# Kernel optimization log

Measured on AMD Instinct MI355X. Metric: run time of the kernel, lower is better.

Reference implementation:

```python
import jax, jax.numpy as jnp
import numpy as np

N, E = 50000, 800000
IN_C, OUT_C, HEADS = 128, 16, 8
EDGE_DIM = 1
NEG_SLOPE = 0.2
LN_EPS = 1e-5


def setup_inputs() -> dict:
    key = jax.random.key(0)
    ks = jax.random.split(key, 12)
    s = 1.0 / np.sqrt(IN_C)
    HC = OUT_C * HEADS
    return {
        "x": jax.random.normal(ks[0], (N, IN_C), jnp.float32),
        "edge_index": jax.random.randint(ks[1], (2, E), 0, N, jnp.int32),
        "edge_attr": jax.random.normal(ks[2], (E, EDGE_DIM), jnp.float32),
        "W": jax.random.normal(ks[3], (IN_C, HC), jnp.float32) * s,
        "b": jnp.zeros((HC,), jnp.float32),
        "att_src": jax.random.normal(ks[4], (HEADS, OUT_C), jnp.float32) * s,
        "att_dst": jax.random.normal(ks[5], (HEADS, OUT_C), jnp.float32) * s,
        "att_edge": jax.random.normal(ks[6], (HEADS, OUT_C), jnp.float32) * s,
        "lin_edge_w": jax.random.normal(ks[7], (EDGE_DIM, HC), jnp.float32) * s,
        "lin_edge_b": jnp.zeros((HC,), jnp.float32),
        "gamma": jnp.ones((HC,), jnp.float32),
        "beta": jnp.zeros((HC,), jnp.float32),
    }


def _segment_softmax(logits, seg, num_segments):
    # numerically-stable softmax over edges grouped by destination node
    m = jax.ops.segment_max(logits, seg, num_segments=num_segments)
    ex = jnp.exp(logits - m[seg])
    z = jax.ops.segment_sum(ex, seg, num_segments=num_segments)
    return ex / (z[seg] + 1e-16)


def reference(x, edge_index, edge_attr, W, b, att_src, att_dst, att_edge,
              lin_edge_w, lin_edge_b, gamma, beta):
    n = x.shape[0]
    src, dst = edge_index[0], edge_index[1]
    # GAT conv: per-head transform, edge-indexed attention, segment softmax, scatter-add
    h = (x @ W).reshape(n, HEADS, OUT_C)                      # [N,H,C]
    a_src = jnp.einsum('nhc,hc->nh', h, att_src)              # [N,H]
    a_dst = jnp.einsum('nhc,hc->nh', h, att_dst)
    e = (edge_attr @ lin_edge_w + lin_edge_b).reshape(-1, HEADS, OUT_C)
    a_edge = jnp.einsum('ehc,hc->eh', e, att_edge)            # [E,H]
    logits = jax.nn.leaky_relu(a_src[src] + a_dst[dst] + a_edge, NEG_SLOPE)
    alpha = _segment_softmax(logits, dst, n)                  # [E,H]
    msg = alpha[..., None] * h[src]                           # [E,H,C]
    out = jax.ops.segment_sum(msg, dst, num_segments=n).reshape(n, -1) + b
    # residual (in_channels == heads*out_channels -> identity projection)
    out = out + x
    # LayerNorm + ELU (dropout is eval-mode identity)
    mu = jnp.mean(out, axis=-1, keepdims=True)
    var = jnp.var(out, axis=-1, keepdims=True)
    out = (out - mu) * jax.lax.rsqrt(var + LN_EPS) * gamma + beta
    return jax.nn.elu(out)
```

## Files before the change

### kernel.cpp

```cpp
#include <hip/hip_runtime.h>
#include <hip/hip_bf16.h>

#define N_NODES 50000
#define N_EDGES 800000
#define IN_C 128
#define HC 128
#define HEADS 8
#define NEG_SLOPE 0.2f
#define LN_EPS 1e-5f

#define LDH 136
#define ELL_CAP 64
#define CNT_STRIDE 16
#define GEMM_BLOCKS 782
#define FILL_BLOCKS 782
#define FUSED_BLOCKS (GEMM_BLOCKS + FILL_BLOCKS)

typedef __hip_bfloat16 bf16;
typedef __attribute__((ext_vector_type(8))) short short8;
typedef __attribute__((ext_vector_type(4))) float f32x4;

__device__ __forceinline__ float b2f(bf16 v) { return __bfloat162float(v); }

__device__ __forceinline__ unsigned short f2bf(float f) {
    unsigned u = __float_as_uint(f);
    return (unsigned short)((u + 0x7fffu + ((u >> 16) & 1u)) >> 16);
}
__device__ __forceinline__ float bf2f(unsigned s) {
    return __uint_as_float(s << 16);
}
__device__ __forceinline__ short8 pack8(float4 u, float4 v) {
    short8 r;
    r[0] = (short)f2bf(u.x); r[1] = (short)f2bf(u.y);
    r[2] = (short)f2bf(u.z); r[3] = (short)f2bf(u.w);
    r[4] = (short)f2bf(v.x); r[5] = (short)f2bf(v.y);
    r[6] = (short)f2bf(v.z); r[7] = (short)f2bf(v.w);
    return r;
}

__global__ __launch_bounds__(256) void prep(
    const float* __restrict__ W, unsigned short* __restrict__ Wt,
    int* __restrict__ cnt)
{
    int id = blockIdx.x * 256 + threadIdx.x;
    int k = id >> 7, n = id & 127;
    Wt[n * 128 + k] = f2bf(W[id]);
    const int4 z4 = make_int4(0, 0, 0, 0);
    int4* c4 = reinterpret_cast<int4*>(cnt);
    const int total4 = N_NODES * CNT_STRIDE / 4;
    for (int j = id; j < total4; j += 64 * 256) c4[j] = z4;
}

__global__ __launch_bounds__(256) void fused(
    const float* __restrict__ x, const unsigned short* __restrict__ Wt,
    const float* __restrict__ att_src, const float* __restrict__ att_dst,
    const int* __restrict__ ei, const float* __restrict__ edge_attr,
    int* __restrict__ cnt, unsigned int* __restrict__ ellp,
    unsigned short* __restrict__ h_out,
    float* __restrict__ a_src, float* __restrict__ a_dst)
{
    __shared__ short sH[4][16 * LDH];
    const int bid = blockIdx.x;
    const int t   = threadIdx.x;

    if (bid & 1) {
        const int fid = bid >> 1;
        const int e0  = (fid * 256 + t) * 4;
        if (e0 >= N_EDGES) return;
        const int4   s4 = *reinterpret_cast<const int4*>(ei + e0);
        const int4   d4 = *reinterpret_cast<const int4*>(ei + N_EDGES + e0);
        const float4 a4 = *reinterpret_cast<const float4*>(edge_attr + e0);

        int p0 = atomicAdd(&cnt[d4.x * CNT_STRIDE], 1);
        int p1 = atomicAdd(&cnt[d4.y * CNT_STRIDE], 1);
        int p2 = atomicAdd(&cnt[d4.z * CNT_STRIDE], 1);
        int p3 = atomicAdd(&cnt[d4.w * CNT_STRIDE], 1);
        if (p0 < ELL_CAP)
            ellp[(d4.x << 6) + p0] = (((unsigned)s4.x) << 16) | (unsigned)f2bf(a4.x);
        if (p1 < ELL_CAP)
            ellp[(d4.y << 6) + p1] = (((unsigned)s4.y) << 16) | (unsigned)f2bf(a4.y);
        if (p2 < ELL_CAP)
            ellp[(d4.z << 6) + p2] = (((unsigned)s4.z) << 16) | (unsigned)f2bf(a4.z);
        if (p3 < ELL_CAP)
            ellp[(d4.w << 6) + p3] = (((unsigned)s4.w) << 16) | (unsigned)f2bf(a4.w);
        return;
    }

    const int gid = bid >> 1;
    const int wv  = t >> 6;
    const int l   = t & 63;
    const int gw  = gid * 4 + wv;
    if (gw >= N_NODES / 16) return;

    const int n0   = gw * 16;
    const int mrow = l & 15;
    const int quad = l >> 4;

    short8 afrag[4];
    const float* xr = x + (size_t)(n0 + mrow) * IN_C + quad * 8;
#pragma unroll
    for (int ko = 0; ko < 4; ++ko) {
        float4 u = *reinterpret_cast<const float4*>(xr + ko * 32);
        float4 v = *reinterpret_cast<const float4*>(xr + ko * 32 + 4);
        afrag[ko] = pack8(u, v);
    }

    f32x4 acc[8];
#pragma unroll
    for (int nt = 0; nt < 8; ++nt) acc[nt] = (f32x4)0.f;
#pragma unroll
    for (int nt = 0; nt < 8; ++nt) {
        const unsigned short* wr = Wt + (nt * 16 + mrow) * 128 + quad * 8;
#pragma unroll
        for (int ko = 0; ko < 4; ++ko) {
            short8 bfr = *reinterpret_cast<const short8*>(wr + ko * 32);
            acc[nt] = __builtin_amdgcn_mfma_f32_16x16x32_bf16(afrag[ko], bfr, acc[nt], 0, 0, 0);
        }
    }

#pragma unroll
    for (int nt = 0; nt < 8; ++nt)
#pragma unroll
        for (int r = 0; r < 4; ++r)
            sH[wv][(quad * 4 + r) * LDH + nt * 16 + mrow] = (short)f2bf(acc[nt][r]);

#pragma unroll
    for (int i = 0; i < 4; ++i) {
        int row = i * 4 + (l >> 4);
        int col = (l & 15) * 8;
        short8 hv = *reinterpret_cast<const short8*>(&sH[wv][row * LDH + col]);
        *reinterpret_cast<short8*>(h_out + (size_t)(n0 + row) * HC + col) = hv;
    }

#pragma unroll
    for (int pp = 0; pp < 2; ++pp) {
        int p  = l + pp * 64;
        int m  = p >> 3;
        int hd = p & 7;
        float ssum = 0.f, dsum = 0.f;
#pragma unroll
        for (int c = 0; c < 16; ++c) {
            float hv = bf2f((unsigned short)sH[wv][m * LDH + hd * 16 + c]);
            ssum = fmaf(hv, att_src[hd * 16 + c], ssum);
            dsum = fmaf(hv, att_dst[hd * 16 + c], dsum);
        }
        a_src[(n0 + m) * HEADS + hd] = ssum;
        a_dst[(n0 + m) * HEADS + hd] = dsum;
    }
}

__global__ __launch_bounds__(256) void gather_node(
    const int* __restrict__ cnt, const unsigned int* __restrict__ ellp,
    const float* __restrict__ a_src, const float* __restrict__ a_dst,
    const bf16* __restrict__ h,
    const float* __restrict__ x, const float* __restrict__ bvec,
    const float* __restrict__ gamma, const float* __restrict__ beta,
    const float* __restrict__ att_edge, const float* __restrict__ lin_w,
    const float* __restrict__ lin_b,
    float* __restrict__ out)
{
    const int wave = threadIdx.x >> 6;
    const int l    = threadIdx.x & 63;
    const int n    = blockIdx.x * 4 + wave;
    const int hh   = l >> 3;
    const int jj   = l & 7;

    float ae0 = att_edge[2 * l], ae1 = att_edge[2 * l + 1];
    float p = ae0 * lin_w[2 * l] + ae1 * lin_w[2 * l + 1];
    float q = ae0 * lin_b[2 * l] + ae1 * lin_b[2 * l + 1];
#pragma unroll
    for (int off = 1; off <= 4; off <<= 1) {
        p += __shfl_xor(p, off, 64);
        q += __shfl_xor(q, off, 64);
    }
    const float2 bv = *reinterpret_cast<const float2*>(bvec + 2 * l);
    const float2 gv = *reinterpret_cast<const float2*>(gamma + 2 * l);
    const float2 be = *reinterpret_cast<const float2*>(beta + 2 * l);

    const float ad  = a_dst[n * HEADS + hh];
    const int   beg = n << 6;
    const int   cn  = min(cnt[n * CNT_STRIDE], ELL_CAP);
    const int   full = cn & ~7;

    float zp = 0.f, acc0 = 0.f, acc1 = 0.f;
    const __hip_bfloat162* h2 = reinterpret_cast<const __hip_bfloat162*>(h);

    if (full > 0) {
        unsigned ce_c = ellp[beg + jj];
        float    as_c = a_src[(ce_c >> 16) * HEADS + hh];

        for (int bs = 0; bs < full; bs += 8) {
            const unsigned ce = ce_c;
            const float    as = as_c;
            ce_c = ellp[beg + bs + 8 + jj];

            const int   sl = ce >> 16;
            const float ea = bf2f(ce & 0xffffu);
            float lg = as + ad + ea * p + q;
            lg = lg > 0.f ? lg : NEG_SLOPE * lg;
            const float ev = __expf(lg);
            zp += ev;
            const int pk = (sl << 16) | (int)f2bf(ev);

            as_c = a_src[(ce_c >> 16) * HEADS + hh];

#define GSTEP(OFF)                                                        \
            {                                                             \
                int pj = __builtin_amdgcn_ds_swizzle(pk, OFF);            \
                int sj = ((unsigned)pj) >> 16;                            \
                float evj = bf2f((unsigned)pj & 0xffffu);                 \
                __hip_bfloat162 hv = h2[(size_t)sj * 64 + l];             \
                acc0 += evj * b2f(hv.x);                                  \
                acc1 += evj * b2f(hv.y);                                  \
            }
            GSTEP(24)  GSTEP(56)  GSTEP(88)  GSTEP(120)
            GSTEP(152) GSTEP(184) GSTEP(216) GSTEP(248)
#undef GSTEP
        }
    }

    const int rem = cn - full;
    if (rem > 0) {
        int sl = 0; float ev = 0.f;
        if (jj < rem) {
            unsigned ce = ellp[beg + full + jj];
            sl = ce >> 16;
            float ea = bf2f(ce & 0xffffu);
            float lg = a_src[sl * HEADS + hh] + ad + ea * p + q;
            lg = lg > 0.f ? lg : NEG_SLOPE * lg;
            ev = __expf(lg);
        }
        zp += ev;
        const int gbase = l & 56;
        for (int j = 0; j < rem; ++j) {
            float evj = __shfl(ev, gbase | j, 64);
            int   sj  = __shfl(sl, gbase | j, 64);
            __hip_bfloat162 hv = h2[(size_t)sj * 64 + l];
            acc0 += evj * b2f(hv.x);
            acc1 += evj * b2f(hv.y);
        }
    }

    float z = zp;
    z += __shfl_xor(z, 1, 64);
    z += __shfl_xor(z, 2, 64);
    z += __shfl_xor(z, 4, 64);
    const float rz = 1.f / (z + 1e-16f);
    acc0 *= rz;
    acc1 *= rz;

    const size_t idx = (size_t)n * HC + 2 * l;
    const float2 xv = *reinterpret_cast<const float2*>(x + idx);
    float v0 = acc0 + xv.x + bv.x;
    float v1 = acc1 + xv.y + bv.y;
    float s1 = v0 + v1, s2 = v0 * v0 + v1 * v1;
#pragma unroll
    for (int off = 32; off >= 1; off >>= 1) {
        s1 += __shfl_xor(s1, off, 64);
        s2 += __shfl_xor(s2, off, 64);
    }
    const float mean = s1 * (1.f / HC);
    const float var  = s2 * (1.f / HC) - mean * mean;
    const float inv  = rsqrtf(var + LN_EPS);
    float y0 = (v0 - mean) * inv * gv.x + be.x;
    float y1 = (v1 - mean) * inv * gv.y + be.y;
    y0 = y0 > 0.f ? y0 : expm1f(y0);
    y1 = y1 > 0.f ? y1 : expm1f(y1);
    *reinterpret_cast<float2*>(out + idx) = make_float2(y0, y1);
}

extern "C" void kernel_launch(void* const* d_in, const int* in_sizes, int n_in,
                              void* d_out, int out_size, void* d_ws, size_t ws_size,
                              hipStream_t stream)
{
    const float* x         = (const float*)d_in[0];
    const int*   ei        = (const int*)d_in[1];
    const float* edge_attr = (const float*)d_in[2];
    const float* W         = (const float*)d_in[3];
    const float* b         = (const float*)d_in[4];
    const float* att_src   = (const float*)d_in[5];
    const float* att_dst   = (const float*)d_in[6];
    const float* att_edge  = (const float*)d_in[7];
    const float* lin_w     = (const float*)d_in[8];
    const float* lin_b     = (const float*)d_in[9];
    const float* gamma     = (const float*)d_in[10];
    const float* beta      = (const float*)d_in[11];

    char* ws = (char*)d_ws;
    bf16*  h     = (bf16*)ws;  ws += (size_t)N_NODES * HC * sizeof(bf16);
    float* a_src = (float*)ws; ws += (size_t)N_NODES * HEADS * sizeof(float);
    float* a_dst = (float*)ws; ws += (size_t)N_NODES * HEADS * sizeof(float);
    int*   cnt   = (int*)ws;   ws += (size_t)N_NODES * CNT_STRIDE * sizeof(int);
    unsigned short* Wt = (unsigned short*)ws;
    ws += (size_t)128 * 128 * sizeof(unsigned short);
    unsigned int* ellp = (unsigned int*)ws;
    ws += (size_t)(N_NODES * ELL_CAP + 64) * sizeof(unsigned int);

    prep<<<64, 256, 0, stream>>>(W, Wt, cnt);

    fused<<<FUSED_BLOCKS, 256, 0, stream>>>(
        x, Wt, att_src, att_dst, ei, edge_attr, cnt, ellp,
        (unsigned short*)h, a_src, a_dst);

    gather_node<<<N_NODES / 4, 256, 0, stream>>>(
        cnt, ellp, a_src, a_dst, h, x, b, gamma, beta,
        att_edge, lin_w, lin_b, (float*)d_out);
}
```

Measured before the change: 192.7 us.

## Split fused GEMM/fill kernel into separate fill and GEMM launches

Replaces the interleaved fused kernel, where odd blocks did edge ELL fill and even blocks did the node GEMM, with two separate kernels launched back to back on the same stream. The fill kernel now handles 8 edges per thread with half as many blocks and uses nontemporal stores for the ELL entries. The aim is to remove the branch divergence and LDS over-allocation that fill blocks carried, and to raise memory-level parallelism per thread. In exchange it adds a launch and gives up the concurrent overlap of atomic-bound fill work with compute-bound GEMM work.

```diff
diff --git a/kernel.cpp b/kernel.cpp
--- a/kernel.cpp
+++ b/kernel.cpp
@@ -13,8 +13,7 @@
 #define ELL_CAP 64
 #define CNT_STRIDE 16
 #define GEMM_BLOCKS 782
-#define FILL_BLOCKS 782
-#define FUSED_BLOCKS (GEMM_BLOCKS + FILL_BLOCKS)
+#define FILL_BLOCKS 391
 
 typedef __hip_bfloat16 bf16;
 typedef __attribute__((ext_vector_type(8))) short short8;
@@ -51,45 +50,56 @@
     for (int j = id; j < total4; j += 64 * 256) c4[j] = z4;
 }
 
-__global__ __launch_bounds__(256) void fused(
+__global__ __launch_bounds__(256) void fill_k(
+    const int* __restrict__ ei, const float* __restrict__ edge_attr,
+    int* __restrict__ cnt, unsigned int* __restrict__ ellp)
+{
+    const int tid = blockIdx.x * 256 + threadIdx.x;
+    const int e0  = tid * 8;
+    if (e0 >= N_EDGES) return;
+    const int4   sa = *reinterpret_cast<const int4*>(ei + e0);
+    const int4   sb = *reinterpret_cast<const int4*>(ei + e0 + 4);
+    const int4   da = *reinterpret_cast<const int4*>(ei + N_EDGES + e0);
+    const int4   db = *reinterpret_cast<const int4*>(ei + N_EDGES + e0 + 4);
+    const float4 aa = *reinterpret_cast<const float4*>(edge_attr + e0);
+    const float4 ab = *reinterpret_cast<const float4*>(edge_attr + e0 + 4);
+
+    int p0 = atomicAdd(&cnt[da.x * CNT_STRIDE], 1);
+    int p1 = atomicAdd(&cnt[da.y * CNT_STRIDE], 1);
+    int p2 = atomicAdd(&cnt[da.z * CNT_STRIDE], 1);
+    int p3 = atomicAdd(&cnt[da.w * CNT_STRIDE], 1);
+    int p4 = atomicAdd(&cnt[db.x * CNT_STRIDE], 1);
+    int p5 = atomicAdd(&cnt[db.y * CNT_STRIDE], 1);
+    int p6 = atomicAdd(&cnt[db.z * CNT_STRIDE], 1);
+    int p7 = atomicAdd(&cnt[db.w * CNT_STRIDE], 1);
+
+#define PUT(P, D, S, A)                                                    \
+    if ((P) < ELL_CAP)                                                     \
+        __builtin_nontemporal_store(                                       \
+            (((unsigned)(S)) << 16) | (unsigned)f2bf(A),                   \
+            &ellp[((D) << 6) + (P)]);
+    PUT(p0, da.x, sa.x, aa.x)
+    PUT(p1, da.y, sa.y, aa.y)
+    PUT(p2, da.z, sa.z, aa.z)
+    PUT(p3, da.w, sa.w, aa.w)
+    PUT(p4, db.x, sb.x, ab.x)
+    PUT(p5, db.y, sb.y, ab.y)
+    PUT(p6, db.z, sb.z, ab.z)
+    PUT(p7, db.w, sb.w, ab.w)
+#undef PUT
+}
+
+__global__ __launch_bounds__(256) void gemm_k(
     const float* __restrict__ x, const unsigned short* __restrict__ Wt,
     const float* __restrict__ att_src, const float* __restrict__ att_dst,
-    const int* __restrict__ ei, const float* __restrict__ edge_attr,
-    int* __restrict__ cnt, unsigned int* __restrict__ ellp,
     unsigned short* __restrict__ h_out,
     float* __restrict__ a_src, float* __restrict__ a_dst)
 {
     __shared__ short sH[4][16 * LDH];
-    const int bid = blockIdx.x;
-    const int t   = threadIdx.x;
-
-    if (bid & 1) {
-        const int fid = bid >> 1;
-        const int e0  = (fid * 256 + t) * 4;
-        if (e0 >= N_EDGES) return;
-        const int4   s4 = *reinterpret_cast<const int4*>(ei + e0);
-        const int4   d4 = *reinterpret_cast<const int4*>(ei + N_EDGES + e0);
-        const float4 a4 = *reinterpret_cast<const float4*>(edge_attr + e0);
-
-        int p0 = atomicAdd(&cnt[d4.x * CNT_STRIDE], 1);
-        int p1 = atomicAdd(&cnt[d4.y * CNT_STRIDE], 1);
-        int p2 = atomicAdd(&cnt[d4.z * CNT_STRIDE], 1);
-        int p3 = atomicAdd(&cnt[d4.w * CNT_STRIDE], 1);
-        if (p0 < ELL_CAP)
-            ellp[(d4.x << 6) + p0] = (((unsigned)s4.x) << 16) | (unsigned)f2bf(a4.x);
-        if (p1 < ELL_CAP)
-            ellp[(d4.y << 6) + p1] = (((unsigned)s4.y) << 16) | (unsigned)f2bf(a4.y);
-        if (p2 < ELL_CAP)
-            ellp[(d4.z << 6) + p2] = (((unsigned)s4.z) << 16) | (unsigned)f2bf(a4.z);
-        if (p3 < ELL_CAP)
-            ellp[(d4.w << 6) + p3] = (((unsigned)s4.w) << 16) | (unsigned)f2bf(a4.w);
-        return;
-    }
-
-    const int gid = bid >> 1;
-    const int wv  = t >> 6;
-    const int l   = t & 63;
-    const int gw  = gid * 4 + wv;
+    const int t  = threadIdx.x;
+    const int wv = t >> 6;
+    const int l  = t & 63;
+    const int gw = blockIdx.x * 4 + wv;
     if (gw >= N_NODES / 16) return;
 
     const int n0   = gw * 16;
@@ -298,9 +308,10 @@
 
     prep<<<64, 256, 0, stream>>>(W, Wt, cnt);
 
-    fused<<<FUSED_BLOCKS, 256, 0, stream>>>(
-        x, Wt, att_src, att_dst, ei, edge_attr, cnt, ellp,
-        (unsigned short*)h, a_src, a_dst);
+    fill_k<<<FILL_BLOCKS, 256, 0, stream>>>(ei, edge_attr, cnt, ellp);
+
+    gemm_k<<<GEMM_BLOCKS, 256, 0, stream>>>(
+        x, Wt, att_src, att_dst, (unsigned short*)h, a_src, a_dst);
 
     gather_node<<<N_NODES / 4, 256, 0, stream>>>(
         cnt, ellp, a_src, a_dst, h, x, b, gamma, beta,
```

Result: slower. 218.0 us (+13.1%).
